# Optimization experiments

Measured on AMD Instinct MI355X. Metric: run time of the kernel, lower is better.

## Reference

```python
import jax, jax.numpy as jnp
import numpy as np

N_NODES = 50000
N_EDGES = 800000
NODE_IN = 64
EDGE_IN = 64
MSG = 64
NODE_OUT = 64
EDGE_OUT = 64
DIM = 2


def setup_inputs() -> dict:
    key = jax.random.key(0)
    ks = jax.random.split(key, 12)
    x = jax.random.normal(ks[0], (N_NODES, NODE_IN), dtype=jnp.float32)
    edge_index = jax.random.randint(ks[1], (2, N_EDGES), 0, N_NODES, dtype=jnp.int64)
    edge_attr = jax.random.normal(ks[2], (N_EDGES, EDGE_IN), dtype=jnp.float32)
    r = jax.random.normal(ks[3], (N_EDGES, DIM), dtype=jnp.float32)
    # reference distances must be positive (divided by in strain computation)
    d_init = jax.random.uniform(ks[4], (N_EDGES, 1), dtype=jnp.float32, minval=0.5, maxval=1.5)
    msg_in = 1 + 2 * NODE_IN + EDGE_IN  # strain(1) + x_j + x_i + edge_attr
    W_msg = jax.random.normal(ks[5], (msg_in, MSG), dtype=jnp.float32) / np.sqrt(msg_in)
    b_msg = jnp.zeros((MSG,), dtype=jnp.float32)
    upd_in = NODE_IN + MSG
    W_upd = jax.random.normal(ks[6], (upd_in, NODE_OUT), dtype=jnp.float32) / np.sqrt(upd_in)
    b_upd = jnp.zeros((NODE_OUT,), dtype=jnp.float32)
    W_edge = jax.random.normal(ks[7], (MSG, EDGE_OUT), dtype=jnp.float32) / np.sqrt(MSG)
    b_edge = jnp.zeros((EDGE_OUT,), dtype=jnp.float32)
    return {"x": x, "edge_index": edge_index, "edge_attr": edge_attr, "r": r,
            "d_init": d_init, "W_msg": W_msg, "b_msg": b_msg, "W_upd": W_upd,
            "b_upd": b_upd, "W_edge": W_edge, "b_edge": b_edge}


def reference(x, edge_index, edge_attr, r, d_init, W_msg, b_msg, W_upd, b_upd, W_edge, b_edge):
    # PyG source_to_target flow: x_j = source = edge_index[0], x_i = target = edge_index[1]
    src = edge_index[0]
    dst = edge_index[1]
    n = x.shape[0]
    d = jnp.linalg.norm(r, axis=-1, keepdims=True)          # [e,1]
    strain = (d - d_init) / d_init                          # [e,1]
    # message: Linear(concat(x_j, x_i, strain, edge_attr)) -> Softplus
    feat = jnp.concatenate([x[src], x[dst], strain, edge_attr], axis=1)  # [e, 1+2*node_in+edge_in]
    msg = jax.nn.softplus(feat @ W_msg + b_msg)             # [e, msg]
    # mean aggregation over incoming edges per target node
    agg = jax.ops.segment_sum(msg, dst, num_segments=n)     # [n, msg]
    cnt = jax.ops.segment_sum(jnp.ones((msg.shape[0], 1), msg.dtype), dst, num_segments=n)
    agg = agg / jnp.maximum(cnt, 1.0)
    # node update: Linear(concat(x, aggr_out))
    x_new = jnp.concatenate([x, agg], axis=1) @ W_upd + b_upd  # [n, node_out]
    # edge update: Linear(messages)
    edge_new = msg @ W_edge + b_edge                        # [e, edge_out]
    return (x_new, edge_new, msg, strain)
```

## Files before the change

### kernel.cpp

```cpp
#include <hip/hip_runtime.h>
#include <math.h>

#define NN 50000
#define NE 800000
#define NTILE 12500
#define NBLK 196

typedef __bf16 bf16x4 __attribute__((ext_vector_type(4)));
typedef __bf16 bf16x8 __attribute__((ext_vector_type(8)));
typedef float  f32x4  __attribute__((ext_vector_type(4)));

__device__ __forceinline__ float softplus_f(float v) {
    const float t = __expf(-fabsf(v));
    return fmaxf(v, 0.f) + __logf(1.f + t);
}

__global__ void k_zero(int* deg) {
    int i = blockIdx.x * blockDim.x + threadIdx.x;
    if (i < NN) deg[i] = 0;
}

__global__ void k_hist(const int* __restrict__ ei, int* __restrict__ deg) {
    int e = blockIdx.x * blockDim.x + threadIdx.x;
    if (e < NE) atomicAdd(&deg[ei[NE + e]], 1);
}

__global__ void k_bsum(const int* __restrict__ deg, int* __restrict__ bsum) {
    __shared__ int ws4[4];
    const int tid = threadIdx.x;
    const int i = blockIdx.x * 256 + tid;
    int v = (i < NN) ? deg[i] : 0;
    #pragma unroll
    for (int off = 1; off < 64; off <<= 1) v += __shfl_xor(v, off);
    if ((tid & 63) == 0) ws4[tid >> 6] = v;
    __syncthreads();
    if (tid == 0) bsum[blockIdx.x] = ws4[0] + ws4[1] + ws4[2] + ws4[3];
}

__global__ void k_bscan(const int* __restrict__ bsum, int* __restrict__ boff) {
    __shared__ int wsum[4];
    const int tid = threadIdx.x, lane = tid & 63, wid = tid >> 6;
    const int v = (tid < NBLK) ? bsum[tid] : 0;
    int s = v;
    #pragma unroll
    for (int off = 1; off < 64; off <<= 1) {
        int t = __shfl_up(s, off);
        if (lane >= off) s += t;
    }
    if (lane == 63) wsum[wid] = s;
    __syncthreads();
    int add = 0;
    #pragma unroll
    for (int q = 0; q < 4; ++q) add += (q < wid) ? wsum[q] : 0;
    if (tid < NBLK) boff[tid] = (s + add) - v;
}

__global__ void k_apply(const int* __restrict__ deg, const int* __restrict__ boff,
                        int* __restrict__ rowptr, int* __restrict__ cursor) {
    __shared__ int wsum[4];
    const int tid = threadIdx.x, lane = tid & 63, wid = tid >> 6;
    const int i = blockIdx.x * 256 + tid;
    const int v = (i < NN) ? deg[i] : 0;
    int s = v;
    #pragma unroll
    for (int off = 1; off < 64; off <<= 1) {
        int t = __shfl_up(s, off);
        if (lane >= off) s += t;
    }
    if (lane == 63) wsum[wid] = s;
    __syncthreads();
    int add = boff[blockIdx.x];
    #pragma unroll
    for (int q = 0; q < 4; ++q) add += (q < wid) ? wsum[q] : 0;
    const int incl = s + add;
    if (i < NN) { rowptr[i + 1] = incl; cursor[i] = incl - v; }
    if (i == 0) rowptr[0] = 0;
}

__global__ void k_scatter(const int* __restrict__ ei, int* __restrict__ cursor,
                          int* __restrict__ eidx) {
    int e = blockIdx.x * blockDim.x + threadIdx.x;
    if (e < NE) {
        int d = ei[NE + e];
        int p = atomicAdd(&cursor[d], 1);
        eidx[p] = e;
    }
}

__global__ __launch_bounds__(256, 3) void k_edge(
    const float* __restrict__ x, const int* __restrict__ ei,
    const float* __restrict__ ea, const float* __restrict__ r2,
    const float* __restrict__ dinit, const float* __restrict__ Wmsg,
    const float* __restrict__ bmsg, const float* __restrict__ Wedge,
    const float* __restrict__ bedge,
    float* __restrict__ out_edge, float* __restrict__ out_msg,
    float* __restrict__ out_strain)
{
    __shared__ __bf16 sWm[64 * 200];
    __shared__ __bf16 sA [64 * 200];
    __shared__ int   sSrc[64];
    __shared__ int   sDst[64];
    __shared__ float sStrain[64];

    const int tid  = threadIdx.x;
    const int lane = tid & 63;
    const int wid  = tid >> 6;
    const int col  = lane & 15;
    const int quad = lane >> 4;

    {
        const int n = tid & 63, kg = tid >> 6;
        for (int k = kg; k < 192; k += 4) {
            float v = (k < 128) ? Wmsg[k * 64 + n] : Wmsg[(k + 1) * 64 + n];
            sWm[n * 200 + k] = (__bf16)v;
        }
    }
    bf16x8 weF[2][4];
    #pragma unroll
    for (int kc = 0; kc < 2; ++kc)
        #pragma unroll
        for (int nt = 0; nt < 4; ++nt) {
            bf16x8 f;
            #pragma unroll
            for (int j = 0; j < 8; ++j)
                f[j] = (__bf16)Wedge[(kc * 32 + quad * 8 + j) * 64 + nt * 16 + col];
            weF[kc][nt] = f;
        }
    float bm[4], be[4], wst[4];
    #pragma unroll
    for (int nt = 0; nt < 4; ++nt) {
        bm[nt]  = bmsg[nt * 16 + col];
        be[nt]  = bedge[nt * 16 + col];
        wst[nt] = Wmsg[128 * 64 + nt * 16 + col];
    }

    for (int tile = blockIdx.x; tile < NTILE; tile += gridDim.x) {
        const int e0 = tile * 64;
        if (tid < 64) { sSrc[tid] = ei[e0 + tid]; sDst[tid] = ei[NE + e0 + tid]; }
        __syncthreads();

        #pragma unroll
        for (int rr = 0; rr < 4; ++rr) {
            const int i = tid + rr * 256;
            const int e = i >> 4, c = i & 15;
            const f32x4 xj = *(const f32x4*)(x + (size_t)sSrc[e] * 64 + c * 4);
            const f32x4 xi = *(const f32x4*)(x + (size_t)sDst[e] * 64 + c * 4);
            const f32x4 ev = __builtin_nontemporal_load(
                                 (const f32x4*)(ea + (size_t)(e0 + e) * 64 + c * 4));
            bf16x4 a, b, d;
            a[0]=(__bf16)xj[0]; a[1]=(__bf16)xj[1]; a[2]=(__bf16)xj[2]; a[3]=(__bf16)xj[3];
            b[0]=(__bf16)xi[0]; b[1]=(__bf16)xi[1]; b[2]=(__bf16)xi[2]; b[3]=(__bf16)xi[3];
            d[0]=(__bf16)ev[0]; d[1]=(__bf16)ev[1]; d[2]=(__bf16)ev[2]; d[3]=(__bf16)ev[3];
            *(bf16x4*)&sA[e * 200 +       c * 4] = a;
            *(bf16x4*)&sA[e * 200 +  64 + c * 4] = b;
            *(bf16x4*)&sA[e * 200 + 128 + c * 4] = d;
        }
        if (tid < 64) {
            const float rx = r2[(size_t)(e0 + tid) * 2];
            const float ry = r2[(size_t)(e0 + tid) * 2 + 1];
            const float di = dinit[e0 + tid];
            const float st = (sqrtf(rx * rx + ry * ry) - di) / di;
            sStrain[tid] = st;
            __builtin_nontemporal_store(st, &out_strain[e0 + tid]);
        }
        __syncthreads();

        f32x4 acc[4];
        const int r0 = wid * 16 + quad * 4;
        #pragma unroll
        for (int nt = 0; nt < 4; ++nt)
            #pragma unroll
            for (int rg = 0; rg < 4; ++rg)
                acc[nt][rg] = sStrain[r0 + rg] * wst[nt];

        const int abase = (wid * 16 + col) * 200 + quad * 8;
        #pragma unroll
        for (int kc = 0; kc < 6; ++kc) {
            const bf16x8 af = *(const bf16x8*)&sA[abase + kc * 32];
            #pragma unroll
            for (int nt = 0; nt < 4; ++nt) {
                const bf16x8 bfr = *(const bf16x8*)&sWm[(nt * 16 + col) * 200 + kc * 32 + quad * 8];
                acc[nt] = __builtin_amdgcn_mfma_f32_16x16x32_bf16(af, bfr, acc[nt], 0, 0, 0);
            }
        }

        __bf16* A2 = &sA[wid * 16 * 200];
        #pragma unroll
        for (int nt = 0; nt < 4; ++nt) {
            #pragma unroll
            for (int rg = 0; rg < 4; ++rg) {
                const int row = quad * 4 + rg;
                const float sp = softplus_f(acc[nt][rg] + bm[nt]);
                out_msg[(size_t)(e0 + wid * 16 + row) * 64 + nt * 16 + col] = sp;
                A2[row * 88 + nt * 16 + col] = (__bf16)sp;
            }
        }
        __syncthreads();

        f32x4 acc2[4];
        #pragma unroll
        for (int nt = 0; nt < 4; ++nt) acc2[nt] = (f32x4){0.f, 0.f, 0.f, 0.f};
        #pragma unroll
        for (int kc = 0; kc < 2; ++kc) {
            const bf16x8 af = *(const bf16x8*)&A2[col * 88 + kc * 32 + quad * 8];
            #pragma unroll
            for (int nt = 0; nt < 4; ++nt)
                acc2[nt] = __builtin_amdgcn_mfma_f32_16x16x32_bf16(af, weF[kc][nt], acc2[nt], 0, 0, 0);
        }
        #pragma unroll
        for (int nt = 0; nt < 4; ++nt) {
            #pragma unroll
            for (int rg = 0; rg < 4; ++rg) {
                __builtin_nontemporal_store(
                    acc2[nt][rg] + be[nt],
                    &out_edge[(size_t)(e0 + wid * 16 + quad * 4 + rg) * 64 + nt * 16 + col]);
            }
        }
        __syncthreads();
    }
}

__global__ __launch_bounds__(256) void k_node(
    const float* __restrict__ x, const float* __restrict__ msg,
    const int* __restrict__ rowptr, const int* __restrict__ eidx,
    const float* __restrict__ Wupd, const float* __restrict__ bupd,
    float* __restrict__ out_x)
{
    __shared__ float sW[128 * 64];
    const int tid = threadIdx.x;
    for (int i = tid; i < 2048; i += 256)
        ((f32x4*)sW)[i] = ((const f32x4*)Wupd)[i];
    __syncthreads();

    const int lane = tid & 63, wid = tid >> 6;
    const float bu = bupd[lane];

    for (int n = blockIdx.x * 4 + wid; n < NN; n += gridDim.x * 4) {
        const int rs = rowptr[n], ren = rowptr[n + 1];

        float a0 = 0.f, a1 = 0.f, a2 = 0.f, a3 = 0.f;
        int j = rs;
        for (; j + 4 <= ren; j += 4) {
            const int e0 = eidx[j], e1 = eidx[j + 1], e2 = eidx[j + 2], e3 = eidx[j + 3];
            a0 += msg[(size_t)e0 * 64 + lane];
            a1 += msg[(size_t)e1 * 64 + lane];
            a2 += msg[(size_t)e2 * 64 + lane];
            a3 += msg[(size_t)e3 * 64 + lane];
        }
        for (; j < ren; ++j) a0 += msg[(size_t)eidx[j] * 64 + lane];
        const float acc  = (a0 + a1) + (a2 + a3);
        const float mean = acc / fmaxf((float)(ren - rs), 1.f);
        const float xr   = x[(size_t)n * 64 + lane];

        float o = bu;
        #pragma unroll 16
        for (int k = 0; k < 64; ++k)
            o += __shfl(xr, k) * sW[k * 64 + lane];
        #pragma unroll 16
        for (int k = 0; k < 64; ++k)
            o += __shfl(mean, k) * sW[(64 + k) * 64 + lane];

        out_x[(size_t)n * 64 + lane] = o;
    }
}

extern "C" void kernel_launch(void* const* d_in, const int* in_sizes, int n_in,
                              void* d_out, int out_size, void* d_ws, size_t ws_size,
                              hipStream_t stream) {
    const float* x     = (const float*)d_in[0];
    const int*   ei    = (const int*)d_in[1];
    const float* ea    = (const float*)d_in[2];
    const float* r2    = (const float*)d_in[3];
    const float* dinit = (const float*)d_in[4];
    const float* Wmsg  = (const float*)d_in[5];
    const float* bmsg  = (const float*)d_in[6];
    const float* Wupd  = (const float*)d_in[7];
    const float* bupd  = (const float*)d_in[8];
    const float* Wedge = (const float*)d_in[9];
    const float* bedge = (const float*)d_in[10];

    float* out_x      = (float*)d_out;
    float* out_edge   = out_x + (size_t)NN * 64;
    float* out_msg    = out_edge + (size_t)NE * 64;
    float* out_strain = out_msg + (size_t)NE * 64;

    int* deg    = (int*)d_ws;
    int* rowptr = deg + 50176;
    int* cursor = rowptr + 50304;
    int* eidx   = cursor + 50176;
    int* bsum   = eidx + 800000;
    int* boff   = bsum + 256;

    k_zero   <<<196,   256, 0, stream>>>(deg);
    k_hist   <<<3125,  256, 0, stream>>>(ei, deg);
    k_bsum   <<<196,   256, 0, stream>>>(deg, bsum);
    k_bscan  <<<1,     256, 0, stream>>>(bsum, boff);
    k_apply  <<<196,   256, 0, stream>>>(deg, boff, rowptr, cursor);
    k_scatter<<<3125,  256, 0, stream>>>(ei, cursor, eidx);
    k_edge   <<<768,   256, 0, stream>>>(x, ei, ea, r2, dinit, Wmsg, bmsg,
                                         Wedge, bedge, out_edge, out_msg, out_strain);
    k_node   <<<2048,  256, 0, stream>>>(x, out_msg, rowptr, eidx, Wupd, bupd, out_x);
}
```

Measured before the change: 795.9 us.

## Pre-convert node features to bf16 and widen edge tiles to 128 edges

Adds a prep kernel that converts x to a bf16 copy in workspace, so the edge kernel gathers half the bytes per neighbor row with 16-byte loads. The edge kernel now runs 512 threads on 128-edge tiles, loads indices directly instead of staging them in shared memory, and replaces one block barrier with a scheduling barrier, since each wave only reads its own A2 rows. The trade is an extra launch plus a write and read of a 6.4MB buffer, higher LDS use per block (about 76KB), and a dependency on the workspace being large enough. If it is too small, the code falls back to the fp32 gather.

```diff
diff --git a/kernel.cpp b/kernel.cpp
--- a/kernel.cpp
+++ b/kernel.cpp
@@ -3,7 +3,7 @@
 
 #define NN 50000
 #define NE 800000
-#define NTILE 12500
+#define NTILE2 6250
 #define NBLK 196
 
 typedef __bf16 bf16x4 __attribute__((ext_vector_type(4)));
@@ -13,6 +13,16 @@
 __device__ __forceinline__ float softplus_f(float v) {
     const float t = __expf(-fabsf(v));
     return fmaxf(v, 0.f) + __logf(1.f + t);
+}
+
+__global__ void k_prep(const float* __restrict__ x, __bf16* __restrict__ xb) {
+    const int i = blockIdx.x * 256 + threadIdx.x;
+    if (i < NN * 16) {
+        const f32x4 v = *(const f32x4*)(x + (size_t)i * 4);
+        bf16x4 b;
+        b[0]=(__bf16)v[0]; b[1]=(__bf16)v[1]; b[2]=(__bf16)v[2]; b[3]=(__bf16)v[3];
+        *(bf16x4*)(xb + (size_t)i * 4) = b;
+    }
 }
 
 __global__ void k_zero(int* deg) {
@@ -87,8 +97,10 @@
     }
 }
 
-__global__ __launch_bounds__(256, 3) void k_edge(
-    const float* __restrict__ x, const int* __restrict__ ei,
+template<bool USE_XB>
+__global__ __launch_bounds__(512, 2) void k_edge(
+    const float* __restrict__ x, const __bf16* __restrict__ xb,
+    const int* __restrict__ ei,
     const float* __restrict__ ea, const float* __restrict__ r2,
     const float* __restrict__ dinit, const float* __restrict__ Wmsg,
     const float* __restrict__ bmsg, const float* __restrict__ Wedge,
@@ -97,10 +109,8 @@
     float* __restrict__ out_strain)
 {
     __shared__ __bf16 sWm[64 * 200];
-    __shared__ __bf16 sA [64 * 200];
-    __shared__ int   sSrc[64];
-    __shared__ int   sDst[64];
-    __shared__ float sStrain[64];
+    __shared__ __bf16 sA [128 * 200];
+    __shared__ float  sStrain[128];
 
     const int tid  = threadIdx.x;
     const int lane = tid & 63;
@@ -110,7 +120,7 @@
 
     {
         const int n = tid & 63, kg = tid >> 6;
-        for (int k = kg; k < 192; k += 4) {
+        for (int k = kg; k < 192; k += 8) {
             float v = (k < 128) ? Wmsg[k * 64 + n] : Wmsg[(k + 1) * 64 + n];
             sWm[n * 200 + k] = (__bf16)v;
         }
@@ -134,28 +144,46 @@
         wst[nt] = Wmsg[128 * 64 + nt * 16 + col];
     }
 
-    for (int tile = blockIdx.x; tile < NTILE; tile += gridDim.x) {
-        const int e0 = tile * 64;
-        if (tid < 64) { sSrc[tid] = ei[e0 + tid]; sDst[tid] = ei[NE + e0 + tid]; }
-        __syncthreads();
-
-        #pragma unroll
-        for (int rr = 0; rr < 4; ++rr) {
-            const int i = tid + rr * 256;
+    for (int tile = blockIdx.x; tile < NTILE2; tile += gridDim.x) {
+        const int e0 = tile * 128;
+
+        if constexpr (USE_XB) {
+            #pragma unroll
+            for (int it = 0; it < 2; ++it) {
+                const int i = tid + it * 512;
+                const int e = i >> 3, c = i & 7;
+                const int s = ei[e0 + e], d = ei[NE + e0 + e];
+                const bf16x8 vj = *(const bf16x8*)(xb + (size_t)s * 64 + c * 8);
+                const bf16x8 vi = *(const bf16x8*)(xb + (size_t)d * 64 + c * 8);
+                *(bf16x8*)&sA[e * 200 +      c * 8] = vj;
+                *(bf16x8*)&sA[e * 200 + 64 + c * 8] = vi;
+            }
+        } else {
+            #pragma unroll
+            for (int it = 0; it < 4; ++it) {
+                const int i = tid + it * 512;
+                const int e = i >> 4, c = i & 15;
+                const int s = ei[e0 + e], d = ei[NE + e0 + e];
+                const f32x4 xj = *(const f32x4*)(x + (size_t)s * 64 + c * 4);
+                const f32x4 xi = *(const f32x4*)(x + (size_t)d * 64 + c * 4);
+                bf16x4 a, b;
+                a[0]=(__bf16)xj[0]; a[1]=(__bf16)xj[1]; a[2]=(__bf16)xj[2]; a[3]=(__bf16)xj[3];
+                b[0]=(__bf16)xi[0]; b[1]=(__bf16)xi[1]; b[2]=(__bf16)xi[2]; b[3]=(__bf16)xi[3];
+                *(bf16x4*)&sA[e * 200 +      c * 4] = a;
+                *(bf16x4*)&sA[e * 200 + 64 + c * 4] = b;
+            }
+        }
+        #pragma unroll
+        for (int it = 0; it < 4; ++it) {
+            const int i = tid + it * 512;
             const int e = i >> 4, c = i & 15;
-            const f32x4 xj = *(const f32x4*)(x + (size_t)sSrc[e] * 64 + c * 4);
-            const f32x4 xi = *(const f32x4*)(x + (size_t)sDst[e] * 64 + c * 4);
             const f32x4 ev = __builtin_nontemporal_load(
                                  (const f32x4*)(ea + (size_t)(e0 + e) * 64 + c * 4));
-            bf16x4 a, b, d;
-            a[0]=(__bf16)xj[0]; a[1]=(__bf16)xj[1]; a[2]=(__bf16)xj[2]; a[3]=(__bf16)xj[3];
-            b[0]=(__bf16)xi[0]; b[1]=(__bf16)xi[1]; b[2]=(__bf16)xi[2]; b[3]=(__bf16)xi[3];
+            bf16x4 d;
             d[0]=(__bf16)ev[0]; d[1]=(__bf16)ev[1]; d[2]=(__bf16)ev[2]; d[3]=(__bf16)ev[3];
-            *(bf16x4*)&sA[e * 200 +       c * 4] = a;
-            *(bf16x4*)&sA[e * 200 +  64 + c * 4] = b;
             *(bf16x4*)&sA[e * 200 + 128 + c * 4] = d;
         }
-        if (tid < 64) {
+        if (tid < 128) {
             const float rx = r2[(size_t)(e0 + tid) * 2];
             const float ry = r2[(size_t)(e0 + tid) * 2 + 1];
             const float di = dinit[e0 + tid];
@@ -195,7 +223,7 @@
                 A2[row * 88 + nt * 16 + col] = (__bf16)sp;
             }
         }
-        __syncthreads();
+        __builtin_amdgcn_sched_barrier(0);
 
         f32x4 acc2[4];
         #pragma unroll
@@ -284,7 +312,12 @@
     float* out_msg    = out_edge + (size_t)NE * 64;
     float* out_strain = out_msg + (size_t)NE * 64;
 
-    int* deg    = (int*)d_ws;
+    const size_t XB_BYTES  = (size_t)NN * 64 * 2;
+    const size_t CSR_INTS  = 50176 + 50304 + 50176 + 800000 + 256 + 256;
+    const bool   use_xb    = ws_size >= XB_BYTES + CSR_INTS * 4 + 64;
+
+    __bf16* xb  = (__bf16*)d_ws;
+    int*    deg = use_xb ? (int*)((char*)d_ws + XB_BYTES) : (int*)d_ws;
     int* rowptr = deg + 50176;
     int* cursor = rowptr + 50304;
     int* eidx   = cursor + 50176;
@@ -297,7 +330,13 @@
     k_bscan  <<<1,     256, 0, stream>>>(bsum, boff);
     k_apply  <<<196,   256, 0, stream>>>(deg, boff, rowptr, cursor);
     k_scatter<<<3125,  256, 0, stream>>>(ei, cursor, eidx);
-    k_edge   <<<768,   256, 0, stream>>>(x, ei, ea, r2, dinit, Wmsg, bmsg,
-                                         Wedge, bedge, out_edge, out_msg, out_strain);
+    if (use_xb) {
+        k_prep        <<<3125, 256, 0, stream>>>(x, xb);
+        k_edge<true>  <<<512,  512, 0, stream>>>(x, xb, ei, ea, r2, dinit, Wmsg, bmsg,
+                                                 Wedge, bedge, out_edge, out_msg, out_strain);
+    } else {
+        k_edge<false> <<<512,  512, 0, stream>>>(x, nullptr, ei, ea, r2, dinit, Wmsg, bmsg,
+                                                 Wedge, bedge, out_edge, out_msg, out_strain);
+    }
     k_node   <<<2048,  256, 0, stream>>>(x, out_msg, rowptr, eidx, Wupd, bupd, out_x);
 }
```

Measured after the change: 797.8 us. About the same (+0.2%).
